# Performance work log

Hardware: AMD Instinct MI355X
Metric: run time of the kernel (lower is better)

The kernel has to match this reference:

```python
import jax, jax.numpy as jnp
import numpy as np

N = 100000
E = 1600000
IN_F = 128
OUT_F = 64
NEG_SLOPE = 0.2


def setup_inputs() -> dict:
    key = jax.random.key(0)
    k1, k2, k3, k4 = jax.random.split(key, 4)
    h = jax.random.normal(k1, (N, IN_F), dtype=jnp.float32)
    edge_index = jax.random.randint(k2, (2, E), 0, N, dtype=jnp.int64 if jax.config.jax_enable_x64 else jnp.int32)
    # glorot-initialized params (scale ~ sqrt(6/(fan_in+fan_out)))
    ws = float(np.sqrt(6.0 / (IN_F + OUT_F)))
    W = jax.random.uniform(k3, (OUT_F, IN_F), dtype=jnp.float32, minval=-ws, maxval=ws)
    as_ = float(np.sqrt(6.0 / (1 + 2 * OUT_F)))
    a = jax.random.uniform(k4, (1, 2 * OUT_F), dtype=jnp.float32, minval=-as_, maxval=as_)
    return {"h": h, "W": W, "a": a, "edge_index": edge_index}


def reference(h, W, a, edge_index):
    n = h.shape[0]
    f_out = W.shape[0]
    h_lin = h @ W.T  # [N, F_out]
    # add self loops
    loops = jnp.arange(n, dtype=edge_index.dtype)
    row = jnp.concatenate([edge_index[0], loops])  # [E+N]
    col = jnp.concatenate([edge_index[1], loops])
    # cat([h_lin[row], h_lin[col]]) @ a.T == h_lin[row]@a1 + h_lin[col]@a2
    a1 = a[0, :f_out]
    a2 = a[0, f_out:]
    s_src = h_lin @ a1  # [N]
    s_dst = h_lin @ a2  # [N]
    e = s_src[row] + s_dst[col]  # [E+N]
    e = jnp.where(e > 0, e, NEG_SLOPE * e)  # LeakyReLU
    # segment softmax over destination (row); every row appears via self loop
    m = jax.ops.segment_max(e, row, num_segments=n)
    ex = jnp.exp(e - m[row])
    denom = jax.ops.segment_sum(ex, row, num_segments=n)
    alpha = ex / denom[row]
    # scatter-add aggregation
    h_prime = jax.ops.segment_sum(alpha[:, None] * h_lin[col], row, num_segments=n)
    return jax.nn.elu(h_prime)
```

## Files before the change

kernel.cpp:

```cpp
#include <hip/hip_runtime.h>
#include <cstdint>

#define N_NODES 100000
#define E_EDGES 1600000
#define TOTAL_E (E_EDGES + N_NODES)
#define IN_F 128
#define OUT_F 64
#define NEG_SLOPE 0.2f

#define NB   256
#define RPB  391
#define GCAP 8192
#define TILE 4096
#define EPT  (TILE / 256)
#define HALF_R 196
#define CCAP 4608

#define GC_PAD 16

#define BIN_BLOCKS ((TOTAL_E + TILE - 1) / TILE)
#define GEMM_BLOCKS 608
#define FRONT_BLOCKS (BIN_BLOCKS + GEMM_BLOCKS)

typedef __attribute__((ext_vector_type(8))) short short8;
typedef __attribute__((ext_vector_type(4))) float float4v;

__device__ __forceinline__ short bf16_rne(float x) {
  unsigned u = __builtin_bit_cast(unsigned, x);
  unsigned r = u + 0x7FFFu + ((u >> 16) & 1u);
  return (short)(r >> 16);
}
__device__ __forceinline__ float bf16_f(short s) {
  unsigned u = ((unsigned)(unsigned short)s) << 16;
  return __builtin_bit_cast(float, u);
}
__device__ __forceinline__ float bf16u_f(unsigned short s) {
  unsigned u = ((unsigned)s) << 16;
  return __builtin_bit_cast(float, u);
}

__device__ __forceinline__ void gemm_body(
    char* smem, int gbid,
    const float* __restrict__ h, const float* __restrict__ W,
    const float* __restrict__ a, unsigned short* __restrict__ h_lin,
    float* __restrict__ s_src, float* __restrict__ s_dst) {
  short* Whi = (short*)smem;
  short* Wlo = (short*)(smem + 16384);

  const int tid = threadIdx.x;
  for (int i = tid; i < OUT_F * IN_F; i += 256) {
    const int n = i >> 7, k = i & 127;
    const float x = W[i];
    const short hi = bf16_rne(x);
    const short lo = bf16_rne(x - bf16_f(hi));
    const int idx = (((k >> 5) * 4 + (n >> 4)) << 9) |
                    (((((k >> 3) & 3) << 4) | (n & 15)) << 3) | (k & 7);
    Whi[idx] = hi;
    Wlo[idx] = lo;
  }
  __syncthreads();

  const int lane = tid & 63;
  const int m    = lane & 15;
  const int q    = lane >> 4;
  const int wgid = gbid * 4 + (tid >> 6);
  const int nw   = GEMM_BLOCKS * 4;

  float a1v[4], a2v[4];
#pragma unroll
  for (int t = 0; t < 4; ++t) {
    a1v[t] = a[t * 16 + m];
    a2v[t] = a[OUT_F + t * 16 + m];
  }

  for (int tile = wgid; tile < N_NODES / 16; tile += nw) {
    const int row0 = tile * 16;
    float4v acc[4] = {{0.f,0.f,0.f,0.f},{0.f,0.f,0.f,0.f},
                      {0.f,0.f,0.f,0.f},{0.f,0.f,0.f,0.f}};

    const float* hbase = h + (size_t)(row0 + m) * IN_F + q * 8;
#pragma unroll
    for (int ks = 0; ks < 4; ++ks) {
      const float4 f0 = *(const float4*)(hbase + 32 * ks);
      const float4 f1 = *(const float4*)(hbase + 32 * ks + 4);
      float av[8] = {f0.x, f0.y, f0.z, f0.w, f1.x, f1.y, f1.z, f1.w};
      short8 ahi, alo;
#pragma unroll
      for (int j = 0; j < 8; ++j) {
        const short hi = bf16_rne(av[j]);
        ahi[j] = hi;
        alo[j] = bf16_rne(av[j] - bf16_f(hi));
      }
#pragma unroll
      for (int t = 0; t < 4; ++t) {
        const int fb = ((ks * 4 + t) << 9) + lane * 8;
        const short8 bhi = *(const short8*)&Whi[fb];
        const short8 blo = *(const short8*)&Wlo[fb];
        acc[t] = __builtin_amdgcn_mfma_f32_16x16x32_bf16(ahi, bhi, acc[t], 0, 0, 0);
        acc[t] = __builtin_amdgcn_mfma_f32_16x16x32_bf16(ahi, blo, acc[t], 0, 0, 0);
        acc[t] = __builtin_amdgcn_mfma_f32_16x16x32_bf16(alo, bhi, acc[t], 0, 0, 0);
      }
    }

#pragma unroll
    for (int t = 0; t < 4; ++t)
#pragma unroll
      for (int r = 0; r < 4; ++r)
        h_lin[(size_t)(row0 + q * 4 + r) * OUT_F + t * 16 + m] =
            (unsigned short)bf16_rne(acc[t][r]);

#pragma unroll
    for (int r = 0; r < 4; ++r) {
      float p = acc[0][r] * a1v[0] + acc[1][r] * a1v[1] +
                acc[2][r] * a1v[2] + acc[3][r] * a1v[3];
      float qq = acc[0][r] * a2v[0] + acc[1][r] * a2v[1] +
                 acc[2][r] * a2v[2] + acc[3][r] * a2v[3];
#pragma unroll
      for (int o = 1; o < 16; o <<= 1) {
        p  += __shfl_xor(p, o, 64);
        qq += __shfl_xor(qq, o, 64);
      }
      if (m == 0) {
        s_src[row0 + q * 4 + r] = p;
        s_dst[row0 + q * 4 + r] = qq;
      }
    }
  }
}

__device__ __forceinline__ void bin_body(
    char* smem, int bbid,
    const int* __restrict__ ei, int* __restrict__ gcur,
    unsigned* __restrict__ regions) {
  unsigned*      reord  = (unsigned*)smem;
  unsigned char* bktid  = (unsigned char*)(smem + 16384);
  int*           hist   = (int*)(smem + 20480);
  int*           scan_s = (int*)(smem + 21504);
  int*           adj    = (int*)(smem + 22528);
  int*           wsum   = (int*)(smem + 23552);

  const int tid = threadIdx.x;
  const int e0  = bbid * TILE;

  hist[tid] = 0;
  __syncthreads();

  int      myb[EPT];
  unsigned myrec[EPT];
#pragma unroll
  for (int k = 0; k < EPT; ++k) {
    const int e = e0 + k * 256 + tid;
    int b = -1; unsigned rec = 0;
    if (e < TOTAL_E) {
      int r, c;
      if (e < E_EDGES) { r = ei[e]; c = ei[E_EDGES + e]; }
      else             { r = e - E_EDGES; c = r; }
      b = (int)((unsigned)r / RPB);
      rec = ((unsigned)(r - b * RPB) << 17) | (unsigned)c;
      atomicAdd(&hist[b], 1);
    }
    myb[k] = b; myrec[k] = rec;
  }
  __syncthreads();

  const int v = hist[tid];
  int base = 0;
  if (v > 0) base = atomicAdd(&gcur[tid * GC_PAD], v);

  const int lane = tid & 63, w = tid >> 6;
  {
    int incl = v;
#pragma unroll
    for (int o = 1; o < 64; o <<= 1) {
      const int t = __shfl_up(incl, o, 64);
      if (lane >= o) incl += t;
    }
    if (lane == 63) wsum[w] = incl;
    __syncthreads();
    int wpre = 0;
    for (int i = 0; i < w; ++i) wpre += wsum[i];
    scan_s[tid] = wpre + incl - v;
    adj[tid]    = wpre + incl - v;
  }
  __syncthreads();

#pragma unroll
  for (int k = 0; k < EPT; ++k) {
    if (myb[k] >= 0) {
      const int pos = atomicAdd(&adj[myb[k]], 1);
      reord[pos]  = myrec[k];
      bktid[pos]  = (unsigned char)myb[k];
    }
  }
  __syncthreads();

  adj[tid] = base - scan_s[tid];
  __syncthreads();

  const int tilesz = scan_s[NB - 1] + hist[NB - 1];
  for (int i = tid; i < tilesz; i += 256) {
    const int b    = bktid[i];
    const int slot = adj[b] + i;
    if (slot < GCAP) regions[(size_t)b * GCAP + slot] = reord[i];
  }
}

__global__ __launch_bounds__(256) void k_front(
    const float* __restrict__ h, const float* __restrict__ W,
    const float* __restrict__ a, const int* __restrict__ ei,
    unsigned short* __restrict__ h_lin, float* __restrict__ s_src,
    float* __restrict__ s_dst, int* __restrict__ gcur,
    unsigned* __restrict__ regions) {
  __shared__ alignas(16) char smem[32768];
  const int bid   = blockIdx.x;
  const int chunk = bid >> 8;
  const int pos   = bid & 255;
  if (chunk == 0) {
    bin_body(smem, pos, ei, gcur, regions);
  } else if (chunk == 1) {
    if (pos < 160) bin_body(smem, 256 + pos, ei, gcur, regions);
    else           gemm_body(smem, pos - 160, h, W, a, h_lin, s_src, s_dst);
  } else if (chunk == 2) {
    gemm_body(smem, 96 + pos, h, W, a, h_lin, s_src, s_dst);
  } else {
    gemm_body(smem, 352 + pos, h, W, a, h_lin, s_src, s_dst);
  }
}

__global__ __launch_bounds__(1024) void k_agg(
    const unsigned short* __restrict__ h_lin, const float* __restrict__ s_src,
    const float* __restrict__ s_dst, const int* __restrict__ gcur,
    const unsigned* __restrict__ regions, float* __restrict__ out) {
  __shared__ int   cnt[HALF_R];
  __shared__ int   off[HALF_R];
  __shared__ float srcs[HALF_R];
  __shared__ uint2 pairs[CCAP];
  __shared__ int   wsum4[4];

  const int blk  = blockIdx.x;
  const int b    = blk >> 1;
  const int half = blk & 1;
  const int rlo  = half * HALF_R;
  const int hr   = half ? (RPB - HALF_R) : HALF_R;
  const int tid  = threadIdx.x;
  const int row0 = b * RPB + rlo;
  const int m    = min(gcur[b * GC_PAD], GCAP);
  const unsigned* reg = regions + (size_t)b * GCAP;

  for (int i = tid; i < HALF_R; i += 1024) {
    cnt[i]  = 0;
    srcs[i] = (i < hr && row0 + i < N_NODES) ? s_src[row0 + i] : 0.f;
  }
  __syncthreads();

  for (int i = tid; i < m; i += 1024) {
    const int rl = (int)(reg[i] >> 17) - rlo;
    if (rl >= 0 && rl < hr) atomicAdd(&cnt[rl], 1);
  }
  __syncthreads();

  const int lane = tid & 63, wv = tid >> 6;
  int incl = 0, v = 0;
  if (tid < 256) {
    v = (tid < hr) ? cnt[tid] : 0;
    incl = v;
#pragma unroll
    for (int o = 1; o < 64; o <<= 1) {
      const int t = __shfl_up(incl, o, 64);
      if (lane >= o) incl += t;
    }
    if (lane == 63) wsum4[wv] = incl;
  }
  __syncthreads();
  if (tid < hr) {
    int wpre = 0;
    for (int i = 0; i < wv; ++i) wpre += wsum4[i];
    off[tid] = wpre + incl - v;
  }
  __syncthreads();

  for (int i = tid; i < m; i += 1024) {
    const unsigned rec = reg[i];
    const int rl = (int)(rec >> 17) - rlo;
    if (rl >= 0 && rl < hr) {
      const int c = (int)(rec & 0x1FFFFu);
      float e = srcs[rl] + s_dst[c];
      e = e > 0.f ? e : NEG_SLOPE * e;
      const float ex = __expf(e);
      const int pos = atomicAdd(&off[rl], 1);
      if (pos < CCAP) pairs[pos] = make_uint2((unsigned)c, __float_as_uint(ex));
    }
  }
  __syncthreads();

  const int qid = lane >> 4;
  const int f4  = (lane & 15) * 4;
  for (int rl = wv; rl < hr; rl += 16) {
    const int row = row0 + rl;
    if (row >= N_NODES) break;
    const int dcnt  = cnt[rl];
    const int end   = off[rl];
    const int start = end - dcnt;
    const uint2* prow = pairs + start;

    float4v acc = {0.f, 0.f, 0.f, 0.f};
    float dsum = 0.f;
    for (int j = 0; j < dcnt; j += 8) {
      const int ja = j + qid;
      const int jb = j + 4 + qid;
      uint2 pa = make_uint2(0u, 0u), pb = make_uint2(0u, 0u);
      if (ja < dcnt) pa = prow[ja];
      if (jb < dcnt) pb = prow[jb];
      const ushort4 ha = *(const ushort4*)&h_lin[(size_t)pa.x * OUT_F + f4];
      const ushort4 hb = *(const ushort4*)&h_lin[(size_t)pb.x * OUT_F + f4];
      const float ea = __uint_as_float(pa.y);
      const float eb = __uint_as_float(pb.y);
      acc.x = fmaf(ea, bf16u_f(ha.x), acc.x);
      acc.y = fmaf(ea, bf16u_f(ha.y), acc.y);
      acc.z = fmaf(ea, bf16u_f(ha.z), acc.z);
      acc.w = fmaf(ea, bf16u_f(ha.w), acc.w);
      acc.x = fmaf(eb, bf16u_f(hb.x), acc.x);
      acc.y = fmaf(eb, bf16u_f(hb.y), acc.y);
      acc.z = fmaf(eb, bf16u_f(hb.z), acc.z);
      acc.w = fmaf(eb, bf16u_f(hb.w), acc.w);
      dsum += ea + eb;
    }

    acc.x += __shfl_xor(acc.x, 16, 64);
    acc.y += __shfl_xor(acc.y, 16, 64);
    acc.z += __shfl_xor(acc.z, 16, 64);
    acc.w += __shfl_xor(acc.w, 16, 64);
    dsum  += __shfl_xor(dsum, 16, 64);
    acc.x += __shfl_xor(acc.x, 32, 64);
    acc.y += __shfl_xor(acc.y, 32, 64);
    acc.z += __shfl_xor(acc.z, 32, 64);
    acc.w += __shfl_xor(acc.w, 32, 64);
    dsum  += __shfl_xor(dsum, 32, 64);

    if (lane < 16) {
      const float inv = 1.f / dsum;
      float4 o;
      o.x = acc.x * inv; o.y = acc.y * inv;
      o.z = acc.z * inv; o.w = acc.w * inv;
      o.x = o.x > 0.f ? o.x : __expf(o.x) - 1.f;
      o.y = o.y > 0.f ? o.y : __expf(o.y) - 1.f;
      o.z = o.z > 0.f ? o.z : __expf(o.z) - 1.f;
      o.w = o.w > 0.f ? o.w : __expf(o.w) - 1.f;
      *(float4*)&out[(size_t)row * OUT_F + f4] = o;
    }
  }
}

extern "C" void kernel_launch(void* const* d_in, const int* in_sizes, int n_in,
                              void* d_out, int out_size, void* d_ws, size_t ws_size,
                              hipStream_t stream) {
  const float* h  = (const float*)d_in[0];
  const float* W  = (const float*)d_in[1];
  const float* a  = (const float*)d_in[2];
  const int*   ei = (const int*)d_in[3];
  float* out = (float*)d_out;

  unsigned short* h_lin = (unsigned short*)d_ws;
  float* s_src = (float*)(h_lin + (size_t)N_NODES * OUT_F);
  float* s_dst = s_src + N_NODES;
  int*   gcur  = (int*)(s_dst + N_NODES);
  unsigned* regions = (unsigned*)(gcur + NB * GC_PAD);

  hipMemsetAsync(gcur, 0, NB * GC_PAD * sizeof(int), stream);

  k_front<<<FRONT_BLOCKS, 256, 0, stream>>>(h, W, a, ei, h_lin, s_src, s_dst,
                                            gcur, regions);

  k_agg<<<NB * 2, 1024, 0, stream>>>(h_lin, s_src, s_dst, gcur, regions, out);
}
```

Measured before the change: 176.0 us.

## Split fused front kernel into separate linear and binning kernels

Replaces the single k_front kernel, which ran edge binning and the node GEMM side by side in different blocks, with two sequential launches: k_linear (782 blocks) and k_bin. The bin tile is halved to 2048 edges, which doubles the number of bin blocks and shrinks per-block shared memory. This drops the block-index dispatch and the 32KB shared buffer every block reserved, but loses the concurrency between the two workloads and adds a launch.

Measured after the change: 180.0 us. 2.3% more time.

```diff
diff --git a/kernel.cpp b/kernel.cpp
--- a/kernel.cpp
+++ b/kernel.cpp
@@ -11,7 +11,7 @@
 #define NB   256
 #define RPB  391
 #define GCAP 8192
-#define TILE 4096
+#define TILE 2048
 #define EPT  (TILE / 256)
 #define HALF_R 196
 #define CCAP 4608
@@ -19,8 +19,6 @@
 #define GC_PAD 16
 
 #define BIN_BLOCKS ((TOTAL_E + TILE - 1) / TILE)
-#define GEMM_BLOCKS 608
-#define FRONT_BLOCKS (BIN_BLOCKS + GEMM_BLOCKS)
 
 typedef __attribute__((ext_vector_type(8))) short short8;
 typedef __attribute__((ext_vector_type(4))) float float4v;
@@ -39,13 +37,12 @@
   return __builtin_bit_cast(float, u);
 }
 
-__device__ __forceinline__ void gemm_body(
-    char* smem, int gbid,
+__global__ __launch_bounds__(256) void k_linear(
     const float* __restrict__ h, const float* __restrict__ W,
     const float* __restrict__ a, unsigned short* __restrict__ h_lin,
     float* __restrict__ s_src, float* __restrict__ s_dst) {
-  short* Whi = (short*)smem;
-  short* Wlo = (short*)(smem + 16384);
+  __shared__ alignas(16) short Whi[16 * 512];
+  __shared__ alignas(16) short Wlo[16 * 512];
 
   const int tid = threadIdx.x;
   for (int i = tid; i < OUT_F * IN_F; i += 256) {
@@ -63,8 +60,8 @@
   const int lane = tid & 63;
   const int m    = lane & 15;
   const int q    = lane >> 4;
-  const int wgid = gbid * 4 + (tid >> 6);
-  const int nw   = GEMM_BLOCKS * 4;
+  const int wgid = blockIdx.x * 4 + (tid >> 6);
+  const int nw   = gridDim.x * 4;
 
   float a1v[4], a2v[4];
 #pragma unroll
@@ -128,19 +125,18 @@
   }
 }
 
-__device__ __forceinline__ void bin_body(
-    char* smem, int bbid,
+__global__ __launch_bounds__(256) void k_bin(
     const int* __restrict__ ei, int* __restrict__ gcur,
     unsigned* __restrict__ regions) {
-  unsigned*      reord  = (unsigned*)smem;
-  unsigned char* bktid  = (unsigned char*)(smem + 16384);
-  int*           hist   = (int*)(smem + 20480);
-  int*           scan_s = (int*)(smem + 21504);
-  int*           adj    = (int*)(smem + 22528);
-  int*           wsum   = (int*)(smem + 23552);
+  __shared__ unsigned reord[TILE];
+  __shared__ unsigned char bktid[TILE];
+  __shared__ int hist[NB];
+  __shared__ int scan_s[NB];
+  __shared__ int adj[NB];
+  __shared__ int wsum[4];
 
   const int tid = threadIdx.x;
-  const int e0  = bbid * TILE;
+  const int e0  = blockIdx.x * TILE;
 
   hist[tid] = 0;
   __syncthreads();
@@ -202,28 +198,6 @@
     const int b    = bktid[i];
     const int slot = adj[b] + i;
     if (slot < GCAP) regions[(size_t)b * GCAP + slot] = reord[i];
-  }
-}
-
-__global__ __launch_bounds__(256) void k_front(
-    const float* __restrict__ h, const float* __restrict__ W,
-    const float* __restrict__ a, const int* __restrict__ ei,
-    unsigned short* __restrict__ h_lin, float* __restrict__ s_src,
-    float* __restrict__ s_dst, int* __restrict__ gcur,
-    unsigned* __restrict__ regions) {
-  __shared__ alignas(16) char smem[32768];
-  const int bid   = blockIdx.x;
-  const int chunk = bid >> 8;
-  const int pos   = bid & 255;
-  if (chunk == 0) {
-    bin_body(smem, pos, ei, gcur, regions);
-  } else if (chunk == 1) {
-    if (pos < 160) bin_body(smem, 256 + pos, ei, gcur, regions);
-    else           gemm_body(smem, pos - 160, h, W, a, h_lin, s_src, s_dst);
-  } else if (chunk == 2) {
-    gemm_body(smem, 96 + pos, h, W, a, h_lin, s_src, s_dst);
-  } else {
-    gemm_body(smem, 352 + pos, h, W, a, h_lin, s_src, s_dst);
   }
 }
 
@@ -368,8 +342,9 @@
 
   hipMemsetAsync(gcur, 0, NB * GC_PAD * sizeof(int), stream);
 
-  k_front<<<FRONT_BLOCKS, 256, 0, stream>>>(h, W, a, ei, h_lin, s_src, s_dst,
-                                            gcur, regions);
+  k_linear<<<782, 256, 0, stream>>>(h, W, a, h_lin, s_src, s_dst);
+
+  k_bin<<<BIN_BLOCKS, 256, 0, stream>>>(ei, gcur, regions);
 
   k_agg<<<NB * 2, 1024, 0, stream>>>(h_lin, s_src, s_dst, gcur, regions, out);
 }
```

## Use finer 512-bin partitioning so each aggregation block owns its bin

Applied to the files above, without the earlier changes.

Doubles the number of destination bins to 512 with 196 rows each and halves the binning tile size, so each aggregation block reads only its own bin instead of scanning a shared bin and filtering half the records. The binning kernel now handles 512 buckets per tile with a two-pass scan. It also simplifies the front-kernel block assignment to bins first, then GEMM. The tradeoff is more binning blocks, more global cursor atomics, and less coalesced scatter writes per bucket.

Result: slower. 195.2 us (+10.9%).

```diff
diff --git a/kernel.cpp b/kernel.cpp
--- a/kernel.cpp
+++ b/kernel.cpp
@@ -8,13 +8,12 @@
 #define OUT_F 64
 #define NEG_SLOPE 0.2f
 
-#define NB   256
-#define RPB  391
-#define GCAP 8192
-#define TILE 4096
+#define NB_F 512
+#define RPB  196
+#define GCAP 4608
+#define CCAP 4608
+#define TILE 2048
 #define EPT  (TILE / 256)
-#define HALF_R 196
-#define CCAP 4608
 
 #define GC_PAD 16
 
@@ -132,17 +131,18 @@
     char* smem, int bbid,
     const int* __restrict__ ei, int* __restrict__ gcur,
     unsigned* __restrict__ regions) {
-  unsigned*      reord  = (unsigned*)smem;
-  unsigned char* bktid  = (unsigned char*)(smem + 16384);
-  int*           hist   = (int*)(smem + 20480);
-  int*           scan_s = (int*)(smem + 21504);
-  int*           adj    = (int*)(smem + 22528);
-  int*           wsum   = (int*)(smem + 23552);
+  unsigned*       reord  = (unsigned*)smem;
+  unsigned short* bktid  = (unsigned short*)(smem + 8192);
+  int*            hist   = (int*)(smem + 12288);
+  int*            scan_s = (int*)(smem + 14336);
+  int*            adj    = (int*)(smem + 16384);
+  int*            wsum   = (int*)(smem + 18432);
 
   const int tid = threadIdx.x;
   const int e0  = bbid * TILE;
 
   hist[tid] = 0;
+  hist[256 + tid] = 0;
   __syncthreads();
 
   int      myb[EPT];
@@ -163,25 +163,41 @@
   }
   __syncthreads();
 
-  const int v = hist[tid];
-  int base = 0;
-  if (v > 0) base = atomicAdd(&gcur[tid * GC_PAD], v);
+  const int v0 = hist[tid];
+  const int v1 = hist[256 + tid];
+  int base0 = 0, base1 = 0;
+  if (v0 > 0) base0 = atomicAdd(&gcur[tid * GC_PAD], v0);
+  if (v1 > 0) base1 = atomicAdd(&gcur[(256 + tid) * GC_PAD], v1);
 
   const int lane = tid & 63, w = tid >> 6;
-  {
-    int incl = v;
-#pragma unroll
-    for (int o = 1; o < 64; o <<= 1) {
-      const int t = __shfl_up(incl, o, 64);
-      if (lane >= o) incl += t;
-    }
-    if (lane == 63) wsum[w] = incl;
-    __syncthreads();
-    int wpre = 0;
-    for (int i = 0; i < w; ++i) wpre += wsum[i];
-    scan_s[tid] = wpre + incl - v;
-    adj[tid]    = wpre + incl - v;
-  }
+  int incl = v0;
+#pragma unroll
+  for (int o = 1; o < 64; o <<= 1) {
+    const int t = __shfl_up(incl, o, 64);
+    if (lane >= o) incl += t;
+  }
+  if (lane == 63) wsum[w] = incl;
+  __syncthreads();
+  int wpre = 0;
+  for (int i = 0; i < w; ++i) wpre += wsum[i];
+  const int T0  = wsum[0] + wsum[1] + wsum[2] + wsum[3];
+  const int ex0 = wpre + incl - v0;
+  __syncthreads();
+
+  incl = v1;
+#pragma unroll
+  for (int o = 1; o < 64; o <<= 1) {
+    const int t = __shfl_up(incl, o, 64);
+    if (lane >= o) incl += t;
+  }
+  if (lane == 63) wsum[w] = incl;
+  __syncthreads();
+  wpre = 0;
+  for (int i = 0; i < w; ++i) wpre += wsum[i];
+  const int ex1 = T0 + wpre + incl - v1;
+
+  scan_s[tid]       = ex0;  adj[tid]       = ex0;
+  scan_s[256 + tid] = ex1;  adj[256 + tid] = ex1;
   __syncthreads();
 
 #pragma unroll
@@ -189,15 +205,16 @@
     if (myb[k] >= 0) {
       const int pos = atomicAdd(&adj[myb[k]], 1);
       reord[pos]  = myrec[k];
-      bktid[pos]  = (unsigned char)myb[k];
-    }
-  }
-  __syncthreads();
-
-  adj[tid] = base - scan_s[tid];
-  __syncthreads();
-
-  const int tilesz = scan_s[NB - 1] + hist[NB - 1];
+      bktid[pos]  = (unsigned short)myb[k];
+    }
+  }
+  __syncthreads();
+
+  adj[tid]       = base0 - scan_s[tid];
+  adj[256 + tid] = base1 - scan_s[256 + tid];
+  __syncthreads();
+
+  const int tilesz = scan_s[NB_F - 1] + hist[NB_F - 1];
   for (int i = tid; i < tilesz; i += 256) {
     const int b    = bktid[i];
     const int slot = adj[b] + i;
@@ -212,18 +229,11 @@
     float* __restrict__ s_dst, int* __restrict__ gcur,
     unsigned* __restrict__ regions) {
   __shared__ alignas(16) char smem[32768];
-  const int bid   = blockIdx.x;
-  const int chunk = bid >> 8;
-  const int pos   = bid & 255;
-  if (chunk == 0) {
-    bin_body(smem, pos, ei, gcur, regions);
-  } else if (chunk == 1) {
-    if (pos < 160) bin_body(smem, 256 + pos, ei, gcur, regions);
-    else           gemm_body(smem, pos - 160, h, W, a, h_lin, s_src, s_dst);
-  } else if (chunk == 2) {
-    gemm_body(smem, 96 + pos, h, W, a, h_lin, s_src, s_dst);
+  const int bid = blockIdx.x;
+  if (bid < BIN_BLOCKS) {
+    bin_body(smem, bid, ei, gcur, regions);
   } else {
-    gemm_body(smem, 352 + pos, h, W, a, h_lin, s_src, s_dst);
+    gemm_body(smem, bid - BIN_BLOCKS, h, W, a, h_lin, s_src, s_dst);
   }
 }
 
@@ -231,31 +241,29 @@
     const unsigned short* __restrict__ h_lin, const float* __restrict__ s_src,
     const float* __restrict__ s_dst, const int* __restrict__ gcur,
     const unsigned* __restrict__ regions, float* __restrict__ out) {
-  __shared__ int   cnt[HALF_R];
-  __shared__ int   off[HALF_R];
-  __shared__ float srcs[HALF_R];
+  __shared__ int   cnt[RPB];
+  __shared__ int   off[RPB];
+  __shared__ float srcs[RPB];
   __shared__ uint2 pairs[CCAP];
   __shared__ int   wsum4[4];
 
-  const int blk  = blockIdx.x;
-  const int b    = blk >> 1;
-  const int half = blk & 1;
-  const int rlo  = half * HALF_R;
-  const int hr   = half ? (RPB - HALF_R) : HALF_R;
+  const int b    = blockIdx.x;
   const int tid  = threadIdx.x;
-  const int row0 = b * RPB + rlo;
-  const int m    = min(gcur[b * GC_PAD], GCAP);
+  const int row0 = b * RPB;
+  int hr = N_NODES - row0;
+  if (hr > RPB) hr = RPB;
+  if (hr < 0)   hr = 0;
+  const int m = min(gcur[b * GC_PAD], GCAP);
   const unsigned* reg = regions + (size_t)b * GCAP;
 
-  for (int i = tid; i < HALF_R; i += 1024) {
+  for (int i = tid; i < RPB; i += 1024) {
     cnt[i]  = 0;
-    srcs[i] = (i < hr && row0 + i < N_NODES) ? s_src[row0 + i] : 0.f;
+    srcs[i] = (i < hr) ? s_src[row0 + i] : 0.f;
   }
   __syncthreads();
 
   for (int i = tid; i < m; i += 1024) {
-    const int rl = (int)(reg[i] >> 17) - rlo;
-    if (rl >= 0 && rl < hr) atomicAdd(&cnt[rl], 1);
+    atomicAdd(&cnt[reg[i] >> 17], 1);
   }
   __syncthreads();
 
@@ -281,15 +289,13 @@
 
   for (int i = tid; i < m; i += 1024) {
     const unsigned rec = reg[i];
-    const int rl = (int)(rec >> 17) - rlo;
-    if (rl >= 0 && rl < hr) {
-      const int c = (int)(rec & 0x1FFFFu);
-      float e = srcs[rl] + s_dst[c];
-      e = e > 0.f ? e : NEG_SLOPE * e;
-      const float ex = __expf(e);
-      const int pos = atomicAdd(&off[rl], 1);
-      if (pos < CCAP) pairs[pos] = make_uint2((unsigned)c, __float_as_uint(ex));
-    }
+    const int rl = (int)(rec >> 17);
+    const int c  = (int)(rec & 0x1FFFFu);
+    float e = srcs[rl] + s_dst[c];
+    e = e > 0.f ? e : NEG_SLOPE * e;
+    const float ex = __expf(e);
+    const int pos = atomicAdd(&off[rl], 1);
+    if (pos < CCAP) pairs[pos] = make_uint2((unsigned)c, __float_as_uint(ex));
   }
   __syncthreads();
 
@@ -297,7 +303,6 @@
   const int f4  = (lane & 15) * 4;
   for (int rl = wv; rl < hr; rl += 16) {
     const int row = row0 + rl;
-    if (row >= N_NODES) break;
     const int dcnt  = cnt[rl];
     const int end   = off[rl];
     const int start = end - dcnt;
@@ -364,12 +369,12 @@
   float* s_src = (float*)(h_lin + (size_t)N_NODES * OUT_F);
   float* s_dst = s_src + N_NODES;
   int*   gcur  = (int*)(s_dst + N_NODES);
-  unsigned* regions = (unsigned*)(gcur + NB * GC_PAD);
-
-  hipMemsetAsync(gcur, 0, NB * GC_PAD * sizeof(int), stream);
+  unsigned* regions = (unsigned*)(gcur + NB_F * GC_PAD);
+
+  hipMemsetAsync(gcur, 0, NB_F * GC_PAD * sizeof(int), stream);
 
   k_front<<<FRONT_BLOCKS, 256, 0, stream>>>(h, W, a, ei, h_lin, s_src, s_dst,
                                             gcur, regions);
 
-  k_agg<<<NB * 2, 1024, 0, stream>>>(h_lin, s_src, s_dst, gcur, regions, out);
-}
+  k_agg<<<NB_F, 1024, 0, stream>>>(h_lin, s_src, s_dst, gcur, regions, out);
+}
```

## Process each bin in one aggregation block and keep edge records in registers

Applied to the files above, without the earlier changes.

The aggregation kernel previously launched two blocks per bin, each re-reading the whole region and filtering by half. Now a single 1024-thread block handles all 391 rows of a bin, so region records are read from global memory once. Each thread holds up to 8 records and their exp values in registers between the count pass and the placement pass, which removes the second global read and the recomputation. The cost is half as many blocks (256, about one per CU), a larger LDS pairs buffer, and a __syncthreads placed inside a divergent branch.

Result: slower. 183.3 us (+4.1%).

```diff
diff --git a/kernel.cpp b/kernel.cpp
--- a/kernel.cpp
+++ b/kernel.cpp
@@ -11,16 +11,17 @@
 #define NB   256
 #define RPB  391
 #define GCAP 8192
+#define CCAP 8192
 #define TILE 4096
 #define EPT  (TILE / 256)
-#define HALF_R 196
-#define CCAP 4608
 
 #define GC_PAD 16
 
 #define BIN_BLOCKS ((TOTAL_E + TILE - 1) / TILE)
 #define GEMM_BLOCKS 608
 #define FRONT_BLOCKS (BIN_BLOCKS + GEMM_BLOCKS)
+
+#define KREC 8
 
 typedef __attribute__((ext_vector_type(8))) short short8;
 typedef __attribute__((ext_vector_type(4))) float float4v;
@@ -231,64 +232,74 @@
     const unsigned short* __restrict__ h_lin, const float* __restrict__ s_src,
     const float* __restrict__ s_dst, const int* __restrict__ gcur,
     const unsigned* __restrict__ regions, float* __restrict__ out) {
-  __shared__ int   cnt[HALF_R];
-  __shared__ int   off[HALF_R];
-  __shared__ float srcs[HALF_R];
   __shared__ uint2 pairs[CCAP];
-  __shared__ int   wsum4[4];
-
-  const int blk  = blockIdx.x;
-  const int b    = blk >> 1;
-  const int half = blk & 1;
-  const int rlo  = half * HALF_R;
-  const int hr   = half ? (RPB - HALF_R) : HALF_R;
+  __shared__ int   cnt[RPB];
+  __shared__ int   off[RPB];
+  __shared__ float srcs[RPB];
+  __shared__ int   wsum8[8];
+
+  const int b    = blockIdx.x;
   const int tid  = threadIdx.x;
-  const int row0 = b * RPB + rlo;
-  const int m    = min(gcur[b * GC_PAD], GCAP);
+  const int row0 = b * RPB;
+  int hr = N_NODES - row0;
+  if (hr > RPB) hr = RPB;
+  const int m = min(gcur[b * GC_PAD], GCAP);
   const unsigned* reg = regions + (size_t)b * GCAP;
 
-  for (int i = tid; i < HALF_R; i += 1024) {
+  for (int i = tid; i < RPB; i += 1024) {
     cnt[i]  = 0;
-    srcs[i] = (i < hr && row0 + i < N_NODES) ? s_src[row0 + i] : 0.f;
-  }
-  __syncthreads();
-
-  for (int i = tid; i < m; i += 1024) {
-    const int rl = (int)(reg[i] >> 17) - rlo;
-    if (rl >= 0 && rl < hr) atomicAdd(&cnt[rl], 1);
+    srcs[i] = (i < hr) ? s_src[row0 + i] : 0.f;
+  }
+  __syncthreads();
+
+  unsigned mrec[KREC];
+  float    mex[KREC];
+#pragma unroll
+  for (int k = 0; k < KREC; ++k) {
+    const int i = tid + k * 1024;
+    mrec[k] = 0u; mex[k] = 0.f;
+    if (i < m) {
+      const unsigned rec = reg[i];
+      const int rl = (int)(rec >> 17);
+      const int c  = (int)(rec & 0x1FFFFu);
+      float e = srcs[rl] + s_dst[c];
+      e = e > 0.f ? e : NEG_SLOPE * e;
+      mrec[k] = rec | 0x80000000u;
+      mex[k]  = __expf(e);
+      atomicAdd(&cnt[rl], 1);
+    }
   }
   __syncthreads();
 
   const int lane = tid & 63, wv = tid >> 6;
-  int incl = 0, v = 0;
-  if (tid < 256) {
-    v = (tid < hr) ? cnt[tid] : 0;
-    incl = v;
+  if (tid < 512) {
+    const int v = (tid < hr) ? cnt[tid] : 0;
+    int incl = v;
 #pragma unroll
     for (int o = 1; o < 64; o <<= 1) {
       const int t = __shfl_up(incl, o, 64);
       if (lane >= o) incl += t;
     }
-    if (lane == 63) wsum4[wv] = incl;
-  }
-  __syncthreads();
-  if (tid < hr) {
-    int wpre = 0;
-    for (int i = 0; i < wv; ++i) wpre += wsum4[i];
-    off[tid] = wpre + incl - v;
-  }
-  __syncthreads();
-
-  for (int i = tid; i < m; i += 1024) {
-    const unsigned rec = reg[i];
-    const int rl = (int)(rec >> 17) - rlo;
-    if (rl >= 0 && rl < hr) {
-      const int c = (int)(rec & 0x1FFFFu);
-      float e = srcs[rl] + s_dst[c];
-      e = e > 0.f ? e : NEG_SLOPE * e;
-      const float ex = __expf(e);
+    if (lane == 63) wsum8[wv] = incl;
+    __syncthreads();
+    if (tid < hr) {
+      int wpre = 0;
+      for (int i = 0; i < wv; ++i) wpre += wsum8[i];
+      off[tid] = wpre + incl - v;
+    }
+  } else {
+    __syncthreads();
+  }
+  __syncthreads();
+
+#pragma unroll
+  for (int k = 0; k < KREC; ++k) {
+    if (mrec[k] & 0x80000000u) {
+      const unsigned rec = mrec[k] & 0x7FFFFFFFu;
+      const int rl = (int)(rec >> 17);
       const int pos = atomicAdd(&off[rl], 1);
-      if (pos < CCAP) pairs[pos] = make_uint2((unsigned)c, __float_as_uint(ex));
+      if (pos < CCAP)
+        pairs[pos] = make_uint2(rec & 0x1FFFFu, __float_as_uint(mex[k]));
     }
   }
   __syncthreads();
@@ -297,7 +308,6 @@
   const int f4  = (lane & 15) * 4;
   for (int rl = wv; rl < hr; rl += 16) {
     const int row = row0 + rl;
-    if (row >= N_NODES) break;
     const int dcnt  = cnt[rl];
     const int end   = off[rl];
     const int start = end - dcnt;
@@ -371,5 +381,5 @@
   k_front<<<FRONT_BLOCKS, 256, 0, stream>>>(h, W, a, ei, h_lin, s_src, s_dst,
                                             gcur, regions);
 
-  k_agg<<<NB * 2, 1024, 0, stream>>>(h_lin, s_src, s_dst, gcur, regions, out);
-}
+  k_agg<<<NB, 1024, 0, stream>>>(h_lin, s_src, s_dst, gcur, regions, out);
+}
```
